# Kernel optimization log

Hardware: AMD Instinct MI355X
Metric: run time of the kernel (lower is better)

## Reference

```python
import jax, jax.numpy as jnp
import numpy as np


def setup_inputs() -> dict:
    key = jax.random.key(0)
    k1, k2, k3 = jax.random.split(key, 3)
    B, S, D = 8, 1024, 128
    logits = jax.random.normal(k1, (B, S, D), dtype=jnp.float32)
    labels = jax.random.normal(k2, (B, S, D), dtype=jnp.float32)
    # all-valid mask: any fully-padded row would make the softmax row all -inf (NaN),
    # matching the original torch behavior; ones keeps the baseline finite.
    pad_mask = jnp.ones((B, S), dtype=jnp.int32)
    ad_idxs = jax.random.randint(k3, (B, S), 0, 1000, dtype=jnp.int64)
    return {"logits": logits, "labels": labels, "pad_mask": pad_mask, "ad_idxs": ad_idxs}


def reference(logits, labels, pad_mask, ad_idxs):
    B, S, D = logits.shape
    N = B * S
    logits_flat = logits.reshape(N, D)
    labels_flat = labels.reshape(N, D)
    valid = pad_mask.reshape(N).astype(bool)
    ad = ad_idxs.reshape(N)

    # [N, N] pairwise similarity
    sim = logits_flat @ labels_flat.T
    pair_valid = valid[:, None] & valid[None, :]
    sim = jnp.where(pair_valid, sim, -jnp.inf)

    sim_prob = jax.nn.softmax(sim, axis=-1)

    label_mat = ((ad[:, None] == ad[None, :]) & pair_valid).astype(sim_prob.dtype)
    EPS = 1e-12
    pos_loss = -jnp.log2(jnp.clip(sim_prob, EPS)) * label_mat
    loss = pos_loss.sum(axis=-1).mean()
    return loss
```

## Files before the change

### kernel.cpp

```cpp
#include <hip/hip_runtime.h>
#include <math.h>

#define N 8192
#define D 128
#define BM 128
#define BN 64
#define NCHUNK 8
#define COLS_PER_CHUNK (N / NCHUNK)
#define SUBTILES (COLS_PER_CHUNK / BN)
#define MAXPOS 32

#define CLIP_TERM 39.86313713864835f
#define LOG2E     1.4426950408889634f

typedef short bf16x8 __attribute__((ext_vector_type(8)));
typedef float f32x4  __attribute__((ext_vector_type(4)));

static __device__ __forceinline__ unsigned short f2bf(float f) {
    unsigned u = __builtin_bit_cast(unsigned, f);
    u += 0x7FFFu + ((u >> 16) & 1u);
    return (unsigned short)(u >> 16);
}

static __device__ __forceinline__ float exp2_fast(float x) {
    return __builtin_amdgcn_exp2f(x);
}

__global__ void convert_kernel(const float* __restrict__ a,
                               const float* __restrict__ b,
                               unsigned short* __restrict__ A,
                               unsigned short* __restrict__ B,
                               int* __restrict__ cnt,
                               float* __restrict__ l_total,
                               float* __restrict__ out) {
    const int t = blockIdx.x * 256 + threadIdx.x;
    if (t < N) { cnt[t] = 0; l_total[t] = 0.0f; }
    if (t == 0) *out = 0.0f;
    const int ND4 = N * D / 4;
    const bool first = t < ND4;
    float4 v = first ? ((const float4*)a)[t] : ((const float4*)b)[t - ND4];
    if (first) { v.x *= LOG2E; v.y *= LOG2E; v.z *= LOG2E; v.w *= LOG2E; }
    ushort4 o;
    o.x = f2bf(v.x); o.y = f2bf(v.y); o.z = f2bf(v.z); o.w = f2bf(v.w);
    if (first) ((ushort4*)A)[t] = o; else ((ushort4*)B)[t - ND4] = o;
}

__global__ __launch_bounds__(256, 3)
void sim_lse_kernel(const unsigned short* __restrict__ Abf,
                    const unsigned short* __restrict__ Bbf,
                    const int* __restrict__ ad,
                    float* __restrict__ l_total,
                    int* __restrict__ cnt,
                    float* __restrict__ pos_sim) {
    __shared__ short As[BM * 128];
    __shared__ short Bs[BN * 128];

    const int tid = threadIdx.x;
    const int rowBase = blockIdx.x * BM;
    const int chunk = blockIdx.y;
    const int lane = tid & 63;
    const int w = tid >> 6;
    const int quad = lane >> 4;
    const int l16 = lane & 15;
    const int wr = (w >> 1) * 64;
    const int wc = (w & 1) * 32;

    {
        const uint4* src = (const uint4*)(Abf + rowBase * D);
#pragma unroll
        for (int it = 0; it < 8; ++it) {
            const int id = tid + it * 256;
            const int row = id >> 4, c = id & 15;
            const int cs = c ^ (row & 15);
            *(uint4*)&As[(row * 16 + cs) * 8] = src[row * 16 + c];
        }
    }

    int ad_row[16];
#pragma unroll
    for (int rt = 0; rt < 4; ++rt)
#pragma unroll
        for (int reg = 0; reg < 4; ++reg)
            ad_row[rt * 4 + reg] = ad[rowBase + wr + rt * 16 + quad * 4 + reg];

    float l[16];
#pragma unroll
    for (int s = 0; s < 16; ++s) l[s] = 0.0f;

    for (int sub = 0; sub < SUBTILES; ++sub) {
        const int colBase = chunk * COLS_PER_CHUNK + sub * BN;
        __syncthreads();
        {
            const uint4* src = (const uint4*)(Bbf + colBase * D);
#pragma unroll
            for (int it = 0; it < 4; ++it) {
                const int id = tid + it * 256;
                const int row = id >> 4, c = id & 15;
                const int cs = c ^ (row & 15);
                *(uint4*)&Bs[(row * 16 + cs) * 8] = src[row * 16 + c];
            }
        }
        __syncthreads();

        f32x4 acc[4][2];
#pragma unroll
        for (int rt = 0; rt < 4; ++rt) { acc[rt][0] = (f32x4)(0.0f); acc[rt][1] = (f32x4)(0.0f); }

#pragma unroll
        for (int kt = 0; kt < 4; ++kt) {
            const int cs = (kt * 4 + quad) ^ l16;
            bf16x8 af[4], bf2[2];
#pragma unroll
            for (int rt = 0; rt < 4; ++rt)
                af[rt] = *(const bf16x8*)&As[((wr + rt * 16 + l16) * 16 + cs) * 8];
#pragma unroll
            for (int ct = 0; ct < 2; ++ct)
                bf2[ct] = *(const bf16x8*)&Bs[((wc + ct * 16 + l16) * 16 + cs) * 8];
#pragma unroll
            for (int rt = 0; rt < 4; ++rt) {
                acc[rt][0] = __builtin_amdgcn_mfma_f32_16x16x32_bf16(af[rt], bf2[0], acc[rt][0], 0, 0, 0);
                acc[rt][1] = __builtin_amdgcn_mfma_f32_16x16x32_bf16(af[rt], bf2[1], acc[rt][1], 0, 0, 0);
            }
        }

        const int adc0 = ad[colBase + wc + l16];
        const int adc1 = ad[colBase + wc + 16 + l16];

#pragma unroll
        for (int rt = 0; rt < 4; ++rt) {
#pragma unroll
            for (int reg = 0; reg < 4; ++reg) {
                const int s = rt * 4 + reg;
                const float v0 = acc[rt][0][reg];
                const float v1 = acc[rt][1][reg];
                l[s] += exp2_fast(v0) + exp2_fast(v1);
                const int adr = ad_row[s];
                if (adc0 == adr) {
                    const int rg = rowBase + wr + rt * 16 + quad * 4 + reg;
                    const int slot = atomicAdd(&cnt[rg], 1);
                    if (slot < MAXPOS) pos_sim[rg * MAXPOS + slot] = v0;
                }
                if (adc1 == adr) {
                    const int rg = rowBase + wr + rt * 16 + quad * 4 + reg;
                    const int slot = atomicAdd(&cnt[rg], 1);
                    if (slot < MAXPOS) pos_sim[rg * MAXPOS + slot] = v1;
                }
            }
        }
    }

#pragma unroll
    for (int s = 0; s < 16; ++s) {
        float ls = l[s];
#pragma unroll
        for (int off = 1; off < 16; off <<= 1) ls += __shfl_xor(ls, off, 64);
        if (l16 == 0) {
            const int rg = rowBase + wr + (s >> 2) * 16 + quad * 4 + (s & 3);
            atomicAdd(&l_total[rg], ls);
        }
    }
}

__global__ __launch_bounds__(256)
void finalize_kernel(const float* __restrict__ l_total,
                     const int* __restrict__ cnt,
                     const float* __restrict__ pos_sim,
                     float* __restrict__ out) {
    const int i = blockIdx.x * 256 + threadIdx.x;
    const float lse = log2f(l_total[i]);
    const int n = min(cnt[i], MAXPOS);
    float sum = 0.0f;
    for (int k = 0; k < n; ++k)
        sum += fminf(lse - pos_sim[i * MAXPOS + k], CLIP_TERM);

#pragma unroll
    for (int off = 32; off >= 1; off >>= 1) sum += __shfl_xor(sum, off, 64);
    __shared__ float red[4];
    const int lane = threadIdx.x & 63, wid = threadIdx.x >> 6;
    if (lane == 0) red[wid] = sum;
    __syncthreads();
    if (threadIdx.x == 0)
        atomicAdd(out, (red[0] + red[1] + red[2] + red[3]) * (1.0f / (float)N));
}

extern "C" void kernel_launch(void* const* d_in, const int* in_sizes, int n_in,
                              void* d_out, int out_size, void* d_ws, size_t ws_size,
                              hipStream_t stream) {
    const float* logits = (const float*)d_in[0];
    const float* labels = (const float*)d_in[1];
    const int* ad = (const int*)d_in[3];
    float* out = (float*)d_out;

    unsigned short* bfA = (unsigned short*)d_ws;
    unsigned short* bfB = bfA + N * D;
    float* l_total = (float*)(bfB + N * D);
    int* cnt = (int*)(l_total + N);
    float* pos_sim = (float*)(cnt + N);

    convert_kernel<<<2 * N * D / 4 / 256, 256, 0, stream>>>(logits, labels, bfA, bfB,
                                                            cnt, l_total, out);
    dim3 g(N / BM, NCHUNK);
    sim_lse_kernel<<<g, 256, 0, stream>>>(bfA, bfB, ad, l_total, cnt, pos_sim);
    finalize_kernel<<<N / 256, 256, 0, stream>>>(l_total, cnt, pos_sim, out);
}
```

Measured before the change: 131.0 us.

## Double-buffer B tiles via direct global-to-LDS loads with pre-swizzled bf16 layout

The convert kernel now writes the bf16 operands already XOR-swizzled, so the GEMM kernel can copy tiles straight into LDS with async global_load_lds instructions instead of going through registers. B tiles are double-buffered, with the next tile prefetched while the current one is multiplied, which removes one barrier per subtile. The column split is doubled to 16 chunks to raise the block count. The trade-offs are a larger LDS footprint, which cuts occupancy to 2 blocks per CU, and more atomic traffic on l_total.

```diff
diff --git a/kernel.cpp b/kernel.cpp
--- a/kernel.cpp
+++ b/kernel.cpp
@@ -5,7 +5,7 @@
 #define D 128
 #define BM 128
 #define BN 64
-#define NCHUNK 8
+#define NCHUNK 16
 #define COLS_PER_CHUNK (N / NCHUNK)
 #define SUBTILES (COLS_PER_CHUNK / BN)
 #define MAXPOS 32
@@ -24,6 +24,15 @@
 
 static __device__ __forceinline__ float exp2_fast(float x) {
     return __builtin_amdgcn_exp2f(x);
+}
+
+typedef __attribute__((address_space(3))) unsigned int lds_u;
+typedef __attribute__((address_space(1))) const unsigned int gbl_u;
+static __device__ __forceinline__ void gl2lds16(const void* g, void* l) {
+    __builtin_amdgcn_global_load_lds(
+        reinterpret_cast<gbl_u*>(reinterpret_cast<uintptr_t>(g)),
+        reinterpret_cast<lds_u*>(reinterpret_cast<uintptr_t>(l)),
+        16, 0, 0);
 }
 
 __global__ void convert_kernel(const float* __restrict__ a,
@@ -36,16 +45,25 @@
     const int t = blockIdx.x * 256 + threadIdx.x;
     if (t < N) { cnt[t] = 0; l_total[t] = 0.0f; }
     if (t == 0) *out = 0.0f;
-    const int ND4 = N * D / 4;
-    const bool first = t < ND4;
-    float4 v = first ? ((const float4*)a)[t] : ((const float4*)b)[t - ND4];
-    if (first) { v.x *= LOG2E; v.y *= LOG2E; v.z *= LOG2E; v.w *= LOG2E; }
-    ushort4 o;
-    o.x = f2bf(v.x); o.y = f2bf(v.y); o.z = f2bf(v.z); o.w = f2bf(v.w);
-    if (first) ((ushort4*)A)[t] = o; else ((ushort4*)B)[t - ND4] = o;
-}
-
-__global__ __launch_bounds__(256, 3)
+    const int half = N * D / 8;
+    const bool first = t < half;
+    const int u = first ? t : t - half;
+    const int row = u >> 4, chunk = u & 15;
+    const float4* src = first ? (const float4*)a : (const float4*)b;
+    float4 v0 = src[u * 2], v1 = src[u * 2 + 1];
+    if (first) {
+        v0.x *= LOG2E; v0.y *= LOG2E; v0.z *= LOG2E; v0.w *= LOG2E;
+        v1.x *= LOG2E; v1.y *= LOG2E; v1.z *= LOG2E; v1.w *= LOG2E;
+    }
+    union { unsigned short us[8]; uint4 v; } p;
+    p.us[0] = f2bf(v0.x); p.us[1] = f2bf(v0.y); p.us[2] = f2bf(v0.z); p.us[3] = f2bf(v0.w);
+    p.us[4] = f2bf(v1.x); p.us[5] = f2bf(v1.y); p.us[6] = f2bf(v1.z); p.us[7] = f2bf(v1.w);
+    const int dchunk = chunk ^ (row & 15);
+    uint4* dst = first ? (uint4*)A : (uint4*)B;
+    dst[row * 16 + dchunk] = p.v;
+}
+
+__global__ __launch_bounds__(256, 2)
 void sim_lse_kernel(const unsigned short* __restrict__ Abf,
                     const unsigned short* __restrict__ Bbf,
                     const int* __restrict__ ad,
@@ -53,11 +71,11 @@
                     int* __restrict__ cnt,
                     float* __restrict__ pos_sim) {
     __shared__ short As[BM * 128];
-    __shared__ short Bs[BN * 128];
+    __shared__ short Bs[2][BN * 128];
 
     const int tid = threadIdx.x;
     const int rowBase = blockIdx.x * BM;
-    const int chunk = blockIdx.y;
+    const int colBase0 = blockIdx.y * COLS_PER_CHUNK;
     const int lane = tid & 63;
     const int w = tid >> 6;
     const int quad = lane >> 4;
@@ -66,13 +84,21 @@
     const int wc = (w & 1) * 32;
 
     {
-        const uint4* src = (const uint4*)(Abf + rowBase * D);
+        const char* Ag = (const char*)(Abf + (size_t)rowBase * D);
+        char* Al = (char*)As;
 #pragma unroll
         for (int it = 0; it < 8; ++it) {
-            const int id = tid + it * 256;
-            const int row = id >> 4, c = id & 15;
-            const int cs = c ^ (row & 15);
-            *(uint4*)&As[(row * 16 + cs) * 8] = src[row * 16 + c];
+            const int off = (w * 8 + it) * 1024;
+            gl2lds16(Ag + off + lane * 16, Al + off);
+        }
+    }
+    {
+        const char* Bg = (const char*)(Bbf + (size_t)colBase0 * D);
+        char* Bl = (char*)Bs[0];
+#pragma unroll
+        for (int it = 0; it < 4; ++it) {
+            const int off = (w * 4 + it) * 1024;
+            gl2lds16(Bg + off + lane * 16, Bl + off);
         }
     }
 
@@ -88,19 +114,20 @@
     for (int s = 0; s < 16; ++s) l[s] = 0.0f;
 
     for (int sub = 0; sub < SUBTILES; ++sub) {
-        const int colBase = chunk * COLS_PER_CHUNK + sub * BN;
         __syncthreads();
-        {
-            const uint4* src = (const uint4*)(Bbf + colBase * D);
+
+        if (sub + 1 < SUBTILES) {
+            const char* Bg = (const char*)(Bbf + (size_t)(colBase0 + (sub + 1) * BN) * D);
+            char* Bl = (char*)Bs[(sub + 1) & 1];
 #pragma unroll
             for (int it = 0; it < 4; ++it) {
-                const int id = tid + it * 256;
-                const int row = id >> 4, c = id & 15;
-                const int cs = c ^ (row & 15);
-                *(uint4*)&Bs[(row * 16 + cs) * 8] = src[row * 16 + c];
+                const int off = (w * 4 + it) * 1024;
+                gl2lds16(Bg + off + lane * 16, Bl + off);
             }
         }
-        __syncthreads();
+
+        const short* Bcur = Bs[sub & 1];
+        const int colBase = colBase0 + sub * BN;
 
         f32x4 acc[4][2];
 #pragma unroll
@@ -115,7 +142,7 @@
                 af[rt] = *(const bf16x8*)&As[((wr + rt * 16 + l16) * 16 + cs) * 8];
 #pragma unroll
             for (int ct = 0; ct < 2; ++ct)
-                bf2[ct] = *(const bf16x8*)&Bs[((wc + ct * 16 + l16) * 16 + cs) * 8];
+                bf2[ct] = *(const bf16x8*)&Bcur[((wc + ct * 16 + l16) * 16 + cs) * 8];
 #pragma unroll
             for (int rt = 0; rt < 4; ++rt) {
                 acc[rt][0] = __builtin_amdgcn_mfma_f32_16x16x32_bf16(af[rt], bf2[0], acc[rt][0], 0, 0, 0);
@@ -197,7 +224,7 @@
     int* cnt = (int*)(l_total + N);
     float* pos_sim = (float*)(cnt + N);
 
-    convert_kernel<<<2 * N * D / 4 / 256, 256, 0, stream>>>(logits, labels, bfA, bfB,
+    convert_kernel<<<2 * N * D / 8 / 256, 256, 0, stream>>>(logits, labels, bfA, bfB,
                                                             cnt, l_total, out);
     dim3 g(N / BM, NCHUNK);
     sim_lse_kernel<<<g, 256, 0, stream>>>(bfA, bfB, ad, l_total, cnt, pos_sim);
```

Measured after the change: 130.2 us. About the same (-0.7%).

## Drop LDS staging; keep A fragments in registers and stream B from global

Applied to the files above, without the earlier changes.

The similarity kernel no longer stages A and B tiles in shared memory. Each wave holds its 64-row A fragments in registers for the whole run and loads B fragments for each 32-column step straight from global/L2, so no __syncthreads barriers are needed. The grid becomes 32 row blocks of 256 rows by 32 column chunks, and launch bounds drop to 2 blocks per SIMD to leave room for the extra registers. Within a block, B is no longer shared between the waves through LDS, so each wave reloads the same B data from cache. That raises L2/L1 traffic and risks exposed global-load latency, and lower occupancy can hide less of it.

```diff
diff --git a/kernel.cpp b/kernel.cpp
--- a/kernel.cpp
+++ b/kernel.cpp
@@ -3,11 +3,8 @@
 
 #define N 8192
 #define D 128
-#define BM 128
-#define BN 64
-#define NCHUNK 8
-#define COLS_PER_CHUNK (N / NCHUNK)
-#define SUBTILES (COLS_PER_CHUNK / BN)
+#define NCHUNK 32
+#define CHUNK_COLS (N / NCHUNK)
 #define MAXPOS 32
 
 #define CLIP_TERM 39.86313713864835f
@@ -45,86 +42,65 @@
     if (first) ((ushort4*)A)[t] = o; else ((ushort4*)B)[t - ND4] = o;
 }
 
-__global__ __launch_bounds__(256, 3)
+__global__ __launch_bounds__(256, 2)
 void sim_lse_kernel(const unsigned short* __restrict__ Abf,
                     const unsigned short* __restrict__ Bbf,
                     const int* __restrict__ ad,
                     float* __restrict__ l_total,
                     int* __restrict__ cnt,
                     float* __restrict__ pos_sim) {
-    __shared__ short As[BM * 128];
-    __shared__ short Bs[BN * 128];
-
     const int tid = threadIdx.x;
-    const int rowBase = blockIdx.x * BM;
-    const int chunk = blockIdx.y;
     const int lane = tid & 63;
     const int w = tid >> 6;
     const int quad = lane >> 4;
     const int l16 = lane & 15;
-    const int wr = (w >> 1) * 64;
-    const int wc = (w & 1) * 32;
+    const int rowBase = blockIdx.x * 256 + w * 64;
+    const int col0 = blockIdx.y * CHUNK_COLS;
 
-    {
-        const uint4* src = (const uint4*)(Abf + rowBase * D);
+    bf16x8 afr[4][4];
 #pragma unroll
-        for (int it = 0; it < 8; ++it) {
-            const int id = tid + it * 256;
-            const int row = id >> 4, c = id & 15;
-            const int cs = c ^ (row & 15);
-            *(uint4*)&As[(row * 16 + cs) * 8] = src[row * 16 + c];
-        }
-    }
+    for (int rt = 0; rt < 4; ++rt)
+#pragma unroll
+        for (int kt = 0; kt < 4; ++kt)
+            afr[rt][kt] = *(const bf16x8*)((const char*)Abf +
+                (size_t)(rowBase + rt * 16 + l16) * 256 + kt * 64 + quad * 16);
 
     int ad_row[16];
 #pragma unroll
     for (int rt = 0; rt < 4; ++rt)
 #pragma unroll
         for (int reg = 0; reg < 4; ++reg)
-            ad_row[rt * 4 + reg] = ad[rowBase + wr + rt * 16 + quad * 4 + reg];
+            ad_row[rt * 4 + reg] = ad[rowBase + rt * 16 + quad * 4 + reg];
 
     float l[16];
 #pragma unroll
     for (int s = 0; s < 16; ++s) l[s] = 0.0f;
 
-    for (int sub = 0; sub < SUBTILES; ++sub) {
-        const int colBase = chunk * COLS_PER_CHUNK + sub * BN;
-        __syncthreads();
-        {
-            const uint4* src = (const uint4*)(Bbf + colBase * D);
+#pragma unroll 2
+    for (int cs = 0; cs < CHUNK_COLS / 32; ++cs) {
+        const int colBase = col0 + cs * 32;
+        const int adc0 = ad[colBase + l16];
+        const int adc1 = ad[colBase + 16 + l16];
+
+        bf16x8 bfr[2][4];
 #pragma unroll
-            for (int it = 0; it < 4; ++it) {
-                const int id = tid + it * 256;
-                const int row = id >> 4, c = id & 15;
-                const int cs = c ^ (row & 15);
-                *(uint4*)&Bs[(row * 16 + cs) * 8] = src[row * 16 + c];
-            }
-        }
-        __syncthreads();
+        for (int ct = 0; ct < 2; ++ct)
+#pragma unroll
+            for (int kt = 0; kt < 4; ++kt)
+                bfr[ct][kt] = *(const bf16x8*)((const char*)Bbf +
+                    (size_t)(colBase + ct * 16 + l16) * 256 + kt * 64 + quad * 16);
 
         f32x4 acc[4][2];
 #pragma unroll
         for (int rt = 0; rt < 4; ++rt) { acc[rt][0] = (f32x4)(0.0f); acc[rt][1] = (f32x4)(0.0f); }
 
 #pragma unroll
-        for (int kt = 0; kt < 4; ++kt) {
-            const int cs = (kt * 4 + quad) ^ l16;
-            bf16x8 af[4], bf2[2];
-#pragma unroll
-            for (int rt = 0; rt < 4; ++rt)
-                af[rt] = *(const bf16x8*)&As[((wr + rt * 16 + l16) * 16 + cs) * 8];
-#pragma unroll
-            for (int ct = 0; ct < 2; ++ct)
-                bf2[ct] = *(const bf16x8*)&Bs[((wc + ct * 16 + l16) * 16 + cs) * 8];
+        for (int kt = 0; kt < 4; ++kt)
 #pragma unroll
             for (int rt = 0; rt < 4; ++rt) {
-                acc[rt][0] = __builtin_amdgcn_mfma_f32_16x16x32_bf16(af[rt], bf2[0], acc[rt][0], 0, 0, 0);
-                acc[rt][1] = __builtin_amdgcn_mfma_f32_16x16x32_bf16(af[rt], bf2[1], acc[rt][1], 0, 0, 0);
+                acc[rt][0] = __builtin_amdgcn_mfma_f32_16x16x32_bf16(afr[rt][kt], bfr[0][kt], acc[rt][0], 0, 0, 0);
+                acc[rt][1] = __builtin_amdgcn_mfma_f32_16x16x32_bf16(afr[rt][kt], bfr[1][kt], acc[rt][1], 0, 0, 0);
             }
-        }
-
-        const int adc0 = ad[colBase + wc + l16];
-        const int adc1 = ad[colBase + wc + 16 + l16];
 
 #pragma unroll
         for (int rt = 0; rt < 4; ++rt) {
@@ -135,13 +111,13 @@
                 const float v1 = acc[rt][1][reg];
                 l[s] += exp2_fast(v0) + exp2_fast(v1);
                 const int adr = ad_row[s];
-                if (adc0 == adr) {
-                    const int rg = rowBase + wr + rt * 16 + quad * 4 + reg;
+                if (__builtin_expect(adc0 == adr, 0)) {
+                    const int rg = rowBase + rt * 16 + quad * 4 + reg;
                     const int slot = atomicAdd(&cnt[rg], 1);
                     if (slot < MAXPOS) pos_sim[rg * MAXPOS + slot] = v0;
                 }
-                if (adc1 == adr) {
-                    const int rg = rowBase + wr + rt * 16 + quad * 4 + reg;
+                if (__builtin_expect(adc1 == adr, 0)) {
+                    const int rg = rowBase + rt * 16 + quad * 4 + reg;
                     const int slot = atomicAdd(&cnt[rg], 1);
                     if (slot < MAXPOS) pos_sim[rg * MAXPOS + slot] = v1;
                 }
@@ -155,7 +131,7 @@
 #pragma unroll
         for (int off = 1; off < 16; off <<= 1) ls += __shfl_xor(ls, off, 64);
         if (l16 == 0) {
-            const int rg = rowBase + wr + (s >> 2) * 16 + quad * 4 + (s & 3);
+            const int rg = rowBase + (s >> 2) * 16 + quad * 4 + (s & 3);
             atomicAdd(&l_total[rg], ls);
         }
     }
@@ -199,7 +175,7 @@
 
     convert_kernel<<<2 * N * D / 4 / 256, 256, 0, stream>>>(logits, labels, bfA, bfB,
                                                             cnt, l_total, out);
-    dim3 g(N / BM, NCHUNK);
+    dim3 g(N / 256, NCHUNK);
     sim_lse_kernel<<<g, 256, 0, stream>>>(bfA, bfB, ad, l_total, cnt, pos_sim);
     finalize_kernel<<<N / 256, 256, 0, stream>>>(l_total, cnt, pos_sim, out);
 }
```

After: 143.0 us. 1.09x slower.
